# Performance work log

Measured on AMD Instinct MI355X. Metric: run time of the kernel, lower is better.

## Reference

```python
import jax, jax.numpy as jnp
import numpy as np

B, T, D, E, H = 4, 2048, 1024, 8, 1024  # H = hidden_units // num_experts


def setup_inputs() -> dict:
    key = jax.random.key(0)
    ks = jax.random.split(key, 5)
    s = 0.02
    return {
        "x": jax.random.normal(ks[0], (B, T, D), dtype=jnp.float32),
        "Wp": jax.random.normal(ks[1], (D, E), dtype=jnp.float32) * s,
        "bp": jnp.zeros((E,), dtype=jnp.float32),
        "W1": jax.random.normal(ks[2], (E, D, H), dtype=jnp.float32) * s,
        "b1": jnp.zeros((E, H), dtype=jnp.float32),
        "W2": jax.random.normal(ks[3], (E, H, D), dtype=jnp.float32) * s,
        "b2": jnp.zeros((E, D), dtype=jnp.float32),
    }


def reference(x, Wp, bp, W1, b1, W2, b2):
    b, t, d = x.shape
    e = Wp.shape[1]
    xf = x.reshape(-1, d)                       # [N, D]
    logits = xf @ Wp + bp                       # [N, E]
    probs = jax.nn.softmax(logits, axis=-1)     # [N, E]
    expert_chosen = jnp.argmax(probs, axis=-1)  # top-1 routing, [N]
    expert_probs = jnp.take_along_axis(probs, expert_chosen[:, None], axis=-1)  # [N,1]

    # Dense masked dispatch/combine (same math as gather-FFN-scatter; ReLU FFN,
    # dropout_rate=0 so dropout is identity).
    out = jnp.zeros_like(xf)
    for i in range(e):
        h = jax.nn.relu(xf @ W1[i] + b1[i])     # [N, H]
        y = h @ W2[i] + b2[i]                   # [N, D]
        mask = (expert_chosen == i).astype(xf.dtype)[:, None]
        out = out + mask * y

    # probs / probs.detach() == 1 in forward; gradient-routing trick preserved.
    out = out * (expert_probs / jax.lax.stop_gradient(expert_probs))
    return out.reshape(b, t, d), probs.reshape(b, t, e), expert_chosen.reshape(b, t)
```

## Files before the change

kernel.cpp:

```cpp
#include <hip/hip_runtime.h>
#include <stdint.h>

#define N_TOK 8192
#define D_DIM 1024
#define E_NUM 8

typedef float f32x4 __attribute__((ext_vector_type(4)));
typedef __bf16 bf16x8 __attribute__((ext_vector_type(8)));

__device__ __forceinline__ unsigned short f32_to_bf16_bits(float f) {
  union { float f; uint32_t u; } v; v.f = f;
  uint32_t u = v.u;
  uint32_t r = u + 0x7fffu + ((u >> 16) & 1u);
  return (unsigned short)(r >> 16);
}

__device__ __forceinline__ void load_lds16(const void* g, void* l) {
  __builtin_amdgcn_global_load_lds(
      (const __attribute__((address_space(1))) void*)g,
      (__attribute__((address_space(3))) void*)l, 16, 0, 0);
}

__device__ __forceinline__ void transpose_tile(unsigned short (*T)[72],
                                               const float* __restrict__ S,
                                               unsigned short* __restrict__ O,
                                               int r0, int c0, int t) {
  const int rr = t >> 4;
  const int cc = (t & 15) * 4;
#pragma unroll
  for (int p = 0; p < 4; p++) {
    int r = p * 16 + rr;
    float4 v = *reinterpret_cast<const float4*>(S + (size_t)(r0 + r) * 1024 + c0 + cc);
    T[cc + 0][r] = f32_to_bf16_bits(v.x);
    T[cc + 1][r] = f32_to_bf16_bits(v.y);
    T[cc + 2][r] = f32_to_bf16_bits(v.z);
    T[cc + 3][r] = f32_to_bf16_bits(v.w);
  }
  __syncthreads();
#pragma unroll
  for (int p = 0; p < 4; p++) {
    int c = p * 16 + rr;
    ushort4 o = *reinterpret_cast<const ushort4*>(&T[c][cc]);
    *reinterpret_cast<ushort4*>(O + (size_t)(c0 + c) * 1024 + r0 + cc) = o;
  }
}

__global__ __launch_bounds__(256) void wpt_kernel(const float* __restrict__ Wp,
                                                  float* __restrict__ WpT) {
  int i = blockIdx.x * 256 + threadIdx.x;
  int e = i >> 10, d = i & 1023;
  WpT[i] = Wp[(size_t)d * E_NUM + e];
}

__global__ __launch_bounds__(256) void routing_w1t_kernel(
    const float* __restrict__ x, const float* __restrict__ WpT,
    const float* __restrict__ bp, float* __restrict__ probs_out,
    float* __restrict__ chosenF, int* __restrict__ chosen,
    unsigned short* __restrict__ xb,
    const float* __restrict__ W1, unsigned short* __restrict__ W1t) {
  __shared__ __align__(16) unsigned short T[64][72];
  __shared__ __align__(16) float pbuf[4][8];
  if (blockIdx.x >= 2048) {
    const int tb = blockIdx.x - 2048;
    const int e = tb >> 8, rc = tb & 255;
    transpose_tile(T, W1 + ((size_t)e << 20), W1t + ((size_t)e << 20),
                   (rc >> 4) * 64, (rc & 15) * 64, threadIdx.x);
    return;
  }
  const int wave = threadIdx.x >> 6;
  const int lane = threadIdx.x & 63;
  const int token = blockIdx.x * 4 + wave;
  const float* xr = x + (size_t)token * D_DIM;
  unsigned short* xbr = xb + (size_t)token * D_DIM;
  double acc[E_NUM];
#pragma unroll
  for (int e = 0; e < E_NUM; e++) acc[e] = 0.0;
#pragma unroll
  for (int it = 0; it < 4; it++) {
    const int d0 = it * 256 + lane * 4;
    float4 xv = *reinterpret_cast<const float4*>(xr + d0);
    ushort4 o;
    o.x = f32_to_bf16_bits(xv.x);
    o.y = f32_to_bf16_bits(xv.y);
    o.z = f32_to_bf16_bits(xv.z);
    o.w = f32_to_bf16_bits(xv.w);
    *reinterpret_cast<ushort4*>(xbr + d0) = o;
#pragma unroll
    for (int e = 0; e < E_NUM; e++) {
      float4 w = *reinterpret_cast<const float4*>(WpT + (e << 10) + d0);
      acc[e] += (double)xv.x * (double)w.x;
      acc[e] += (double)xv.y * (double)w.y;
      acc[e] += (double)xv.z * (double)w.z;
      acc[e] += (double)xv.w * (double)w.w;
    }
  }
#pragma unroll
  for (int e = 0; e < E_NUM; e++) {
#pragma unroll
    for (int off = 32; off > 0; off >>= 1) acc[e] += __shfl_xor(acc[e], off);
  }
  if (lane == 0) {
    double lg[E_NUM];
#pragma unroll
    for (int e = 0; e < E_NUM; e++) lg[e] = acc[e] + (double)bp[e];
    int best = 0;
    double bv = lg[0];
#pragma unroll
    for (int e = 1; e < E_NUM; e++)
      if (lg[e] > bv) { bv = lg[e]; best = e; }
    double s = 0.0, ex[E_NUM];
#pragma unroll
    for (int e = 0; e < E_NUM; e++) { ex[e] = exp(lg[e] - bv); s += ex[e]; }
    double inv = 1.0 / s;
#pragma unroll
    for (int e = 0; e < E_NUM; e++) pbuf[wave][e] = (float)(ex[e] * inv);
    chosenF[token] = (float)best;
    chosen[token] = best;
  }
  __syncthreads();
  if (threadIdx.x < 8) {
    float4 v = *reinterpret_cast<const float4*>(
        &pbuf[threadIdx.x >> 1][(threadIdx.x & 1) * 4]);
    reinterpret_cast<float4*>(probs_out + (size_t)blockIdx.x * 32)[threadIdx.x] = v;
  }
}

__global__ __launch_bounds__(1024) void scan_scatter_kernel(
    const int* __restrict__ chosen, int* __restrict__ offsets,
    int* __restrict__ perm) {
  __shared__ int hist[E_NUM];
  __shared__ int curs[E_NUM];
  const int t = threadIdx.x;
  if (t < E_NUM) hist[t] = 0;
  __syncthreads();
  for (int n = t; n < N_TOK; n += 1024) atomicAdd(&hist[chosen[n]], 1);
  __syncthreads();
  if (t == 0) {
    int off = 0;
    for (int e = 0; e < E_NUM; e++) { offsets[e] = off; curs[e] = off; off += hist[e]; }
    offsets[E_NUM] = off;
  }
  __syncthreads();
  for (int n = t; n < N_TOK; n += 1024) {
    int e = chosen[n];
    int p = atomicAdd(&curs[e], 1);
    perm[p] = n;
  }
}

__global__ __launch_bounds__(256) void transpose_cast_kernel(
    const float* __restrict__ src, unsigned short* __restrict__ dst) {
  __shared__ __align__(16) unsigned short T[64][72];
  const int e = blockIdx.z;
  transpose_tile(T, src + ((size_t)e << 20), dst + ((size_t)e << 20),
                 blockIdx.y * 64, blockIdx.x * 64, threadIdx.x);
}

template <int MODE>
__global__ __launch_bounds__(256) void moe_gemm_kernel(
    const unsigned short* __restrict__ Abase,
    const unsigned short* __restrict__ Wt,
    const float* __restrict__ bias,
    const int* __restrict__ offsets, const int* __restrict__ perm,
    unsigned short* __restrict__ hb, float* __restrict__ out,
    const float* __restrict__ tsrc, unsigned short* __restrict__ tdst,
    int gemm_blocks) {
  __shared__ __align__(16) unsigned short As[2][128 * 64];
  __shared__ __align__(16) unsigned short Bs[2][64 * 64];

  if ((int)blockIdx.x >= gemm_blocks) {
    const int tb = blockIdx.x - gemm_blocks;
    const int e = tb >> 8, rc = tb & 255;
    auto T = reinterpret_cast<unsigned short(*)[72]>(&As[0][0]);
    transpose_tile(T, tsrc + ((size_t)e << 20), tdst + ((size_t)e << 20),
                   (rc >> 4) * 64, (rc & 15) * 64, threadIdx.x);
    return;
  }

  const int e = blockIdx.x & 7;
  const int slot = blockIdx.x >> 3;
  const int g0 = offsets[e];
  const int m_count = offsets[e + 1] - g0;
  const int m0 = (slot >> 4) * 128;
  if (m0 >= m_count) return;
  const int n0 = (slot & 15) * 64;

  const int tid = threadIdx.x;
  const int wid = tid >> 6, lane = tid & 63;
  const int lrow = lane >> 3;
  const int lchunk = lane & 7;
  const int schunk = lchunk ^ lrow;

  const unsigned short* ga[4];
  const unsigned short* gb[2];
  int abase[4], bbase[2];
  const unsigned short* WtE = Wt + ((size_t)e << 20);
#pragma unroll
  for (int t = 0; t < 4; t++) {
    const int rbase = t * 32 + wid * 8;
    const int r = rbase + lrow;
    int gr = g0 + m0 + r;
    if (gr > N_TOK - 1) gr = N_TOK - 1;
    const int arow = (MODE == 0) ? perm[gr] : gr;
    ga[t] = Abase + (size_t)arow * 1024 + schunk * 8;
    abase[t] = rbase * 64;
  }
#pragma unroll
  for (int t = 0; t < 2; t++) {
    const int rbase = t * 32 + wid * 8;
    const int r = rbase + lrow;
    gb[t] = WtE + (size_t)(n0 + r) * 1024 + schunk * 8;
    bbase[t] = rbase * 64;
  }

  f32x4 acc[4][2];
  const f32x4 zero4 = {0.f, 0.f, 0.f, 0.f};
#pragma unroll
  for (int i = 0; i < 4; i++)
#pragma unroll
    for (int j = 0; j < 2; j++) acc[i][j] = zero4;

  const int wr = wid >> 1, wc = wid & 1;
  const int lr = lane & 15, lk = lane >> 4;

  auto stage = [&](int buf) {
#pragma unroll
    for (int t = 0; t < 4; t++) {
      load_lds16(ga[t], &As[buf][abase[t]]);
      ga[t] += 64;
    }
#pragma unroll
    for (int t = 0; t < 2; t++) {
      load_lds16(gb[t], &Bs[buf][bbase[t]]);
      gb[t] += 64;
    }
  };
  auto compute = [&](int buf) {
#pragma unroll
    for (int kk = 0; kk < 64; kk += 32) {
      bf16x8 af[4], bfr[2];
#pragma unroll
      for (int mf = 0; mf < 4; mf++) {
        const int ra = wr * 64 + mf * 16 + lr;
        const int ca = ((kk >> 3) + lk) ^ (ra & 7);
        af[mf] = *reinterpret_cast<const bf16x8*>(&As[buf][ra * 64 + ca * 8]);
      }
#pragma unroll
      for (int nf = 0; nf < 2; nf++) {
        const int rb = wc * 32 + nf * 16 + lr;
        const int cb = ((kk >> 3) + lk) ^ (rb & 7);
        bfr[nf] = *reinterpret_cast<const bf16x8*>(&Bs[buf][rb * 64 + cb * 8]);
      }
#pragma unroll
      for (int mf = 0; mf < 4; mf++)
#pragma unroll
        for (int nf = 0; nf < 2; nf++)
          acc[mf][nf] = __builtin_amdgcn_mfma_f32_16x16x32_bf16(
              af[mf], bfr[nf], acc[mf][nf], 0, 0, 0);
    }
  };

  stage(0);
  stage(1);
#pragma unroll
  for (int kt = 0; kt < 16; kt++) {
    if (kt < 15) {
      asm volatile("s_waitcnt vmcnt(6)" ::: "memory");
    } else {
      asm volatile("s_waitcnt vmcnt(0)" ::: "memory");
    }
    __builtin_amdgcn_sched_barrier(0);
    __builtin_amdgcn_s_barrier();
    __builtin_amdgcn_s_setprio(1);
    compute(kt & 1);
    __builtin_amdgcn_s_setprio(0);
    __builtin_amdgcn_s_barrier();
    if (kt < 14) stage(kt & 1);
  }

  const int mlim = m_count - m0;
#pragma unroll
  for (int nf = 0; nf < 2; nf++) {
    const int c = n0 + wc * 32 + nf * 16 + lr;
    const float bval = bias[(e << 10) + c];
#pragma unroll
    for (int mf = 0; mf < 4; mf++) {
#pragma unroll
      for (int j = 0; j < 4; j++) {
        const int lrow2 = wr * 64 + mf * 16 + lk * 4 + j;
        if (lrow2 < mlim) {
          float v = acc[mf][nf][j] + bval;
          if (MODE == 0) {
            v = v > 0.f ? v : 0.f;
            hb[(size_t)(g0 + m0 + lrow2) * 1024 + c] = f32_to_bf16_bits(v);
          } else {
            int token = perm[g0 + m0 + lrow2];
            out[(size_t)token * 1024 + c] = v;
          }
        }
      }
    }
  }
}

extern "C" void kernel_launch(void* const* d_in, const int* in_sizes, int n_in,
                              void* d_out, int out_size, void* d_ws, size_t ws_size,
                              hipStream_t stream) {
  const float* x = (const float*)d_in[0];
  const float* Wp = (const float*)d_in[1];
  const float* bp = (const float*)d_in[2];
  const float* W1 = (const float*)d_in[3];
  const float* b1 = (const float*)d_in[4];
  const float* W2 = (const float*)d_in[5];
  const float* b2 = (const float*)d_in[6];

  float* out = (float*)d_out;
  float* probs = out + (size_t)N_TOK * D_DIM;
  float* chosenF = probs + (size_t)N_TOK * E_NUM;

  char* ws = (char*)d_ws;
  int* chosen = (int*)(ws + 0);
  int* perm = (int*)(ws + 32768);
  float* WpT = (float*)(ws + 65536);
  int* offsets = (int*)(ws + 98304);
  const size_t MB16 = 16777216;
  unsigned short* xb = (unsigned short*)(ws + 131072);
  unsigned short* Wt1 = (unsigned short*)(ws + 131072 + MB16);
  const bool overlap = ws_size >= 131072 + 4 * MB16;
  unsigned short* Wt2 = (unsigned short*)(ws + 131072 + (overlap ? 2 : 1) * MB16);
  unsigned short* hb = (unsigned short*)(ws + 131072 + (overlap ? 3 : 2) * MB16);

  const int GEMM_BLOCKS = E_NUM * 64 * 16;

  wpt_kernel<<<32, 256, 0, stream>>>(Wp, WpT);
  routing_w1t_kernel<<<4096, 256, 0, stream>>>(x, WpT, bp, probs, chosenF, chosen,
                                               xb, W1, Wt1);
  scan_scatter_kernel<<<1, 1024, 0, stream>>>(chosen, offsets, perm);
  if (overlap) {
    moe_gemm_kernel<0><<<GEMM_BLOCKS + 2048, 256, 0, stream>>>(
        xb, Wt1, b1, offsets, perm, hb, nullptr, W2, Wt2, GEMM_BLOCKS);
  } else {
    moe_gemm_kernel<0><<<GEMM_BLOCKS, 256, 0, stream>>>(
        xb, Wt1, b1, offsets, perm, hb, nullptr, nullptr, nullptr, GEMM_BLOCKS);
    transpose_cast_kernel<<<dim3(16, 16, 8), 256, 0, stream>>>(W2, Wt2);
  }
  moe_gemm_kernel<1><<<GEMM_BLOCKS, 256, 0, stream>>>(
      hb, Wt2, b2, offsets, perm, nullptr, out, nullptr, nullptr, GEMM_BLOCKS);
}
```

Before: 117.6 us.

## Enlarge MoE GEMM tiles to 256x128 with 8 waves and move W2 transpose

The expert GEMM now uses 512-thread blocks computing 256x128 output tiles, up from 128x64. Each wave holds a 4x4 grid of MFMA accumulators, which raises LDS reuse and cuts redundant global loads of A and B. The W2 transpose/cast is moved out of the first GEMM launch and into the routing kernel's grid, so the GEMM no longer mixes in transpose blocks. The larger tiles use more LDS (about 96KB) and more registers, and they waste more work on the ragged per-expert row counts, with fewer blocks available to fill the GPU.

```diff
diff --git a/kernel.cpp b/kernel.cpp
--- a/kernel.cpp
+++ b/kernel.cpp
@@ -57,9 +57,17 @@
     const float* __restrict__ bp, float* __restrict__ probs_out,
     float* __restrict__ chosenF, int* __restrict__ chosen,
     unsigned short* __restrict__ xb,
-    const float* __restrict__ W1, unsigned short* __restrict__ W1t) {
+    const float* __restrict__ W1, unsigned short* __restrict__ W1t,
+    const float* __restrict__ W2, unsigned short* __restrict__ W2t) {
   __shared__ __align__(16) unsigned short T[64][72];
   __shared__ __align__(16) float pbuf[4][8];
+  if (blockIdx.x >= 4096) {
+    const int tb = blockIdx.x - 4096;
+    const int e = tb >> 8, rc = tb & 255;
+    transpose_tile(T, W2 + ((size_t)e << 20), W2t + ((size_t)e << 20),
+                   (rc >> 4) * 64, (rc & 15) * 64, threadIdx.x);
+    return;
+  }
   if (blockIdx.x >= 2048) {
     const int tb = blockIdx.x - 2048;
     const int e = tb >> 8, rc = tb & 255;
@@ -157,33 +165,22 @@
 }
 
 template <int MODE>
-__global__ __launch_bounds__(256) void moe_gemm_kernel(
+__global__ __launch_bounds__(512, 1) void moe_gemm_kernel(
     const unsigned short* __restrict__ Abase,
     const unsigned short* __restrict__ Wt,
     const float* __restrict__ bias,
     const int* __restrict__ offsets, const int* __restrict__ perm,
-    unsigned short* __restrict__ hb, float* __restrict__ out,
-    const float* __restrict__ tsrc, unsigned short* __restrict__ tdst,
-    int gemm_blocks) {
-  __shared__ __align__(16) unsigned short As[2][128 * 64];
-  __shared__ __align__(16) unsigned short Bs[2][64 * 64];
-
-  if ((int)blockIdx.x >= gemm_blocks) {
-    const int tb = blockIdx.x - gemm_blocks;
-    const int e = tb >> 8, rc = tb & 255;
-    auto T = reinterpret_cast<unsigned short(*)[72]>(&As[0][0]);
-    transpose_tile(T, tsrc + ((size_t)e << 20), tdst + ((size_t)e << 20),
-                   (rc >> 4) * 64, (rc & 15) * 64, threadIdx.x);
-    return;
-  }
+    unsigned short* __restrict__ hb, float* __restrict__ out) {
+  __shared__ __align__(16) unsigned short As[2][256 * 64];
+  __shared__ __align__(16) unsigned short Bs[2][128 * 64];
 
   const int e = blockIdx.x & 7;
   const int slot = blockIdx.x >> 3;
   const int g0 = offsets[e];
   const int m_count = offsets[e + 1] - g0;
-  const int m0 = (slot >> 4) * 128;
+  const int m0 = (slot >> 3) * 256;
   if (m0 >= m_count) return;
-  const int n0 = (slot & 15) * 64;
+  const int n0 = (slot & 7) * 128;
 
   const int tid = threadIdx.x;
   const int wid = tid >> 6, lane = tid & 63;
@@ -197,7 +194,7 @@
   const unsigned short* WtE = Wt + ((size_t)e << 20);
 #pragma unroll
   for (int t = 0; t < 4; t++) {
-    const int rbase = t * 32 + wid * 8;
+    const int rbase = (wid * 4 + t) * 8;
     const int r = rbase + lrow;
     int gr = g0 + m0 + r;
     if (gr > N_TOK - 1) gr = N_TOK - 1;
@@ -207,18 +204,18 @@
   }
 #pragma unroll
   for (int t = 0; t < 2; t++) {
-    const int rbase = t * 32 + wid * 8;
+    const int rbase = (wid * 2 + t) * 8;
     const int r = rbase + lrow;
     gb[t] = WtE + (size_t)(n0 + r) * 1024 + schunk * 8;
     bbase[t] = rbase * 64;
   }
 
-  f32x4 acc[4][2];
+  f32x4 acc[4][4];
   const f32x4 zero4 = {0.f, 0.f, 0.f, 0.f};
 #pragma unroll
   for (int i = 0; i < 4; i++)
 #pragma unroll
-    for (int j = 0; j < 2; j++) acc[i][j] = zero4;
+    for (int j = 0; j < 4; j++) acc[i][j] = zero4;
 
   const int wr = wid >> 1, wc = wid & 1;
   const int lr = lane & 15, lk = lane >> 4;
@@ -238,7 +235,7 @@
   auto compute = [&](int buf) {
 #pragma unroll
     for (int kk = 0; kk < 64; kk += 32) {
-      bf16x8 af[4], bfr[2];
+      bf16x8 af[4], bfr[4];
 #pragma unroll
       for (int mf = 0; mf < 4; mf++) {
         const int ra = wr * 64 + mf * 16 + lr;
@@ -246,15 +243,15 @@
         af[mf] = *reinterpret_cast<const bf16x8*>(&As[buf][ra * 64 + ca * 8]);
       }
 #pragma unroll
-      for (int nf = 0; nf < 2; nf++) {
-        const int rb = wc * 32 + nf * 16 + lr;
+      for (int nf = 0; nf < 4; nf++) {
+        const int rb = wc * 64 + nf * 16 + lr;
         const int cb = ((kk >> 3) + lk) ^ (rb & 7);
         bfr[nf] = *reinterpret_cast<const bf16x8*>(&Bs[buf][rb * 64 + cb * 8]);
       }
 #pragma unroll
       for (int mf = 0; mf < 4; mf++)
 #pragma unroll
-        for (int nf = 0; nf < 2; nf++)
+        for (int nf = 0; nf < 4; nf++)
           acc[mf][nf] = __builtin_amdgcn_mfma_f32_16x16x32_bf16(
               af[mf], bfr[nf], acc[mf][nf], 0, 0, 0);
     }
@@ -280,8 +277,8 @@
 
   const int mlim = m_count - m0;
 #pragma unroll
-  for (int nf = 0; nf < 2; nf++) {
-    const int c = n0 + wc * 32 + nf * 16 + lr;
+  for (int nf = 0; nf < 4; nf++) {
+    const int c = n0 + wc * 64 + nf * 16 + lr;
     const float bval = bias[(e << 10) + c];
 #pragma unroll
     for (int mf = 0; mf < 4; mf++) {
@@ -330,20 +327,17 @@
   unsigned short* Wt2 = (unsigned short*)(ws + 131072 + (overlap ? 2 : 1) * MB16);
   unsigned short* hb = (unsigned short*)(ws + 131072 + (overlap ? 3 : 2) * MB16);
 
-  const int GEMM_BLOCKS = E_NUM * 64 * 16;
+  const int GEMM_BLOCKS = E_NUM * 32 * 8;
 
   wpt_kernel<<<32, 256, 0, stream>>>(Wp, WpT);
-  routing_w1t_kernel<<<4096, 256, 0, stream>>>(x, WpT, bp, probs, chosenF, chosen,
-                                               xb, W1, Wt1);
+  routing_w1t_kernel<<<overlap ? 6144 : 4096, 256, 0, stream>>>(
+      x, WpT, bp, probs, chosenF, chosen, xb, W1, Wt1, W2, Wt2);
   scan_scatter_kernel<<<1, 1024, 0, stream>>>(chosen, offsets, perm);
-  if (overlap) {
-    moe_gemm_kernel<0><<<GEMM_BLOCKS + 2048, 256, 0, stream>>>(
-        xb, Wt1, b1, offsets, perm, hb, nullptr, W2, Wt2, GEMM_BLOCKS);
-  } else {
-    moe_gemm_kernel<0><<<GEMM_BLOCKS, 256, 0, stream>>>(
-        xb, Wt1, b1, offsets, perm, hb, nullptr, nullptr, nullptr, GEMM_BLOCKS);
+  moe_gemm_kernel<0><<<GEMM_BLOCKS, 512, 0, stream>>>(
+      xb, Wt1, b1, offsets, perm, hb, nullptr);
+  if (!overlap) {
     transpose_cast_kernel<<<dim3(16, 16, 8), 256, 0, stream>>>(W2, Wt2);
   }
-  moe_gemm_kernel<1><<<GEMM_BLOCKS, 256, 0, stream>>>(
-      hb, Wt2, b2, offsets, perm, nullptr, out, nullptr, nullptr, GEMM_BLOCKS);
-}
+  moe_gemm_kernel<1><<<GEMM_BLOCKS, 512, 0, stream>>>(
+      hb, Wt2, b2, offsets, perm, nullptr, out);
+}
```

After: 157.8 us. +34.1%, slower.

## Parallelize token scatter per expert and use smaller K tile for first GEMM

Applied to the files above, without the earlier changes.

The single-block scan/scatter is replaced by one block per expert. Each block rebuilds the histogram, computes its own offset and scatters only its expert's tokens, which removes contention on shared cursors. The GEMM kernel is templated on the K-tile size, and the first FFN GEMM uses BK=32 to halve LDS use and possibly raise occupancy. The trade-off is twice as many K iterations and barriers, plus redundant histogram work across the 8 scatter blocks.

```diff
diff --git a/kernel.cpp b/kernel.cpp
--- a/kernel.cpp
+++ b/kernel.cpp
@@ -125,26 +125,33 @@
   }
 }
 
-__global__ __launch_bounds__(1024) void scan_scatter_kernel(
+__global__ __launch_bounds__(256) void scan_scatter_kernel(
     const int* __restrict__ chosen, int* __restrict__ offsets,
     int* __restrict__ perm) {
   __shared__ int hist[E_NUM];
-  __shared__ int curs[E_NUM];
+  __shared__ int cur;
+  const int e = blockIdx.x;
   const int t = threadIdx.x;
   if (t < E_NUM) hist[t] = 0;
   __syncthreads();
-  for (int n = t; n < N_TOK; n += 1024) atomicAdd(&hist[chosen[n]], 1);
+  for (int n = t; n < N_TOK; n += 256) atomicAdd(&hist[chosen[n]], 1);
   __syncthreads();
   if (t == 0) {
     int off = 0;
-    for (int e = 0; e < E_NUM; e++) { offsets[e] = off; curs[e] = off; off += hist[e]; }
-    offsets[E_NUM] = off;
-  }
-  __syncthreads();
-  for (int n = t; n < N_TOK; n += 1024) {
-    int e = chosen[n];
-    int p = atomicAdd(&curs[e], 1);
-    perm[p] = n;
+    for (int i = 0; i < e; i++) off += hist[i];
+    cur = off;
+    if (e == 0) {
+      int o = 0;
+      for (int i = 0; i < E_NUM; i++) { offsets[i] = o; o += hist[i]; }
+      offsets[E_NUM] = o;
+    }
+  }
+  __syncthreads();
+  for (int n = t; n < N_TOK; n += 256) {
+    if (chosen[n] == e) {
+      int p = atomicAdd(&cur, 1);
+      perm[p] = n;
+    }
   }
 }
 
@@ -156,7 +163,7 @@
                  blockIdx.y * 64, blockIdx.x * 64, threadIdx.x);
 }
 
-template <int MODE>
+template <int MODE, int BK>
 __global__ __launch_bounds__(256) void moe_gemm_kernel(
     const unsigned short* __restrict__ Abase,
     const unsigned short* __restrict__ Wt,
@@ -165,8 +172,13 @@
     unsigned short* __restrict__ hb, float* __restrict__ out,
     const float* __restrict__ tsrc, unsigned short* __restrict__ tdst,
     int gemm_blocks) {
-  __shared__ __align__(16) unsigned short As[2][128 * 64];
-  __shared__ __align__(16) unsigned short Bs[2][64 * 64];
+  constexpr int NCH = BK / 8;
+  constexpr int RPL = 64 / NCH;
+  constexpr int ALW = 32 / RPL;
+  constexpr int BLW = 16 / RPL;
+  constexpr int KSTEPS = 1024 / BK;
+  __shared__ __align__(16) unsigned short As[2][128 * BK];
+  __shared__ __align__(16) unsigned short Bs[2][64 * BK];
 
   if ((int)blockIdx.x >= gemm_blocks) {
     const int tb = blockIdx.x - gemm_blocks;
@@ -187,30 +199,30 @@
 
   const int tid = threadIdx.x;
   const int wid = tid >> 6, lane = tid & 63;
-  const int lrow = lane >> 3;
-  const int lchunk = lane & 7;
-  const int schunk = lchunk ^ lrow;
-
-  const unsigned short* ga[4];
-  const unsigned short* gb[2];
-  int abase[4], bbase[2];
+  const int lrow = lane / NCH;
+  const int lchunk = lane & (NCH - 1);
+  const int schunk = lchunk ^ (lrow & (NCH - 1));
+
+  const unsigned short* ga[ALW];
+  const unsigned short* gb[BLW];
+  int abase[ALW], bbase[BLW];
   const unsigned short* WtE = Wt + ((size_t)e << 20);
 #pragma unroll
-  for (int t = 0; t < 4; t++) {
-    const int rbase = t * 32 + wid * 8;
+  for (int t = 0; t < ALW; t++) {
+    const int rbase = (wid * ALW + t) * RPL;
     const int r = rbase + lrow;
     int gr = g0 + m0 + r;
     if (gr > N_TOK - 1) gr = N_TOK - 1;
     const int arow = (MODE == 0) ? perm[gr] : gr;
     ga[t] = Abase + (size_t)arow * 1024 + schunk * 8;
-    abase[t] = rbase * 64;
-  }
-#pragma unroll
-  for (int t = 0; t < 2; t++) {
-    const int rbase = t * 32 + wid * 8;
+    abase[t] = rbase * BK;
+  }
+#pragma unroll
+  for (int t = 0; t < BLW; t++) {
+    const int rbase = (wid * BLW + t) * RPL;
     const int r = rbase + lrow;
     gb[t] = WtE + (size_t)(n0 + r) * 1024 + schunk * 8;
-    bbase[t] = rbase * 64;
+    bbase[t] = rbase * BK;
   }
 
   f32x4 acc[4][2];
@@ -225,31 +237,31 @@
 
   auto stage = [&](int buf) {
 #pragma unroll
-    for (int t = 0; t < 4; t++) {
+    for (int t = 0; t < ALW; t++) {
       load_lds16(ga[t], &As[buf][abase[t]]);
-      ga[t] += 64;
-    }
-#pragma unroll
-    for (int t = 0; t < 2; t++) {
+      ga[t] += BK;
+    }
+#pragma unroll
+    for (int t = 0; t < BLW; t++) {
       load_lds16(gb[t], &Bs[buf][bbase[t]]);
-      gb[t] += 64;
+      gb[t] += BK;
     }
   };
   auto compute = [&](int buf) {
 #pragma unroll
-    for (int kk = 0; kk < 64; kk += 32) {
+    for (int kk = 0; kk < BK; kk += 32) {
       bf16x8 af[4], bfr[2];
 #pragma unroll
       for (int mf = 0; mf < 4; mf++) {
         const int ra = wr * 64 + mf * 16 + lr;
-        const int ca = ((kk >> 3) + lk) ^ (ra & 7);
-        af[mf] = *reinterpret_cast<const bf16x8*>(&As[buf][ra * 64 + ca * 8]);
+        const int ca = ((kk >> 3) + lk) ^ (ra & (NCH - 1));
+        af[mf] = *reinterpret_cast<const bf16x8*>(&As[buf][ra * BK + ca * 8]);
       }
 #pragma unroll
       for (int nf = 0; nf < 2; nf++) {
         const int rb = wc * 32 + nf * 16 + lr;
-        const int cb = ((kk >> 3) + lk) ^ (rb & 7);
-        bfr[nf] = *reinterpret_cast<const bf16x8*>(&Bs[buf][rb * 64 + cb * 8]);
+        const int cb = ((kk >> 3) + lk) ^ (rb & (NCH - 1));
+        bfr[nf] = *reinterpret_cast<const bf16x8*>(&Bs[buf][rb * BK + cb * 8]);
       }
 #pragma unroll
       for (int mf = 0; mf < 4; mf++)
@@ -263,9 +275,12 @@
   stage(0);
   stage(1);
 #pragma unroll
-  for (int kt = 0; kt < 16; kt++) {
-    if (kt < 15) {
-      asm volatile("s_waitcnt vmcnt(6)" ::: "memory");
+  for (int kt = 0; kt < KSTEPS; kt++) {
+    if (kt < KSTEPS - 1) {
+      if constexpr (BK == 64)
+        asm volatile("s_waitcnt vmcnt(6)" ::: "memory");
+      else
+        asm volatile("s_waitcnt vmcnt(3)" ::: "memory");
     } else {
       asm volatile("s_waitcnt vmcnt(0)" ::: "memory");
     }
@@ -275,7 +290,7 @@
     compute(kt & 1);
     __builtin_amdgcn_s_setprio(0);
     __builtin_amdgcn_s_barrier();
-    if (kt < 14) stage(kt & 1);
+    if (kt < KSTEPS - 2) stage(kt & 1);
   }
 
   const int mlim = m_count - m0;
@@ -335,15 +350,15 @@
   wpt_kernel<<<32, 256, 0, stream>>>(Wp, WpT);
   routing_w1t_kernel<<<4096, 256, 0, stream>>>(x, WpT, bp, probs, chosenF, chosen,
                                                xb, W1, Wt1);
-  scan_scatter_kernel<<<1, 1024, 0, stream>>>(chosen, offsets, perm);
+  scan_scatter_kernel<<<E_NUM, 256, 0, stream>>>(chosen, offsets, perm);
   if (overlap) {
-    moe_gemm_kernel<0><<<GEMM_BLOCKS + 2048, 256, 0, stream>>>(
+    moe_gemm_kernel<0, 32><<<GEMM_BLOCKS + 2048, 256, 0, stream>>>(
         xb, Wt1, b1, offsets, perm, hb, nullptr, W2, Wt2, GEMM_BLOCKS);
   } else {
-    moe_gemm_kernel<0><<<GEMM_BLOCKS, 256, 0, stream>>>(
+    moe_gemm_kernel<0, 32><<<GEMM_BLOCKS, 256, 0, stream>>>(
         xb, Wt1, b1, offsets, perm, hb, nullptr, nullptr, nullptr, GEMM_BLOCKS);
     transpose_cast_kernel<<<dim3(16, 16, 8), 256, 0, stream>>>(W2, Wt2);
   }
-  moe_gemm_kernel<1><<<GEMM_BLOCKS, 256, 0, stream>>>(
+  moe_gemm_kernel<1, 64><<<GEMM_BLOCKS, 256, 0, stream>>>(
       hb, Wt2, b2, offsets, perm, nullptr, out, nullptr, nullptr, GEMM_BLOCKS);
 }
```

Measured after the change: 130.5 us. 1.11x slower.
